# Performance work log

Hardware: AMD Instinct MI355X
Metric: run time of the kernel (lower is better)

## Reference

```python
import jax, jax.numpy as jnp
import numpy as np

# Module hyperparameters (from init_kwargs)
KERNEL = (16, 16)     # sliding window shape; Linear in_features = prod = 256
STRIDE = (8, 8)       # window stride
DILATION = (4, 4)     # per-window output tile; Linear out_features = prod = 16
# padding = 0, bias = False (module defaults)


def setup_inputs() -> dict:
    key = jax.random.key(0)
    k1, k2 = jax.random.split(key)
    x = jax.random.normal(k1, (32, 1024, 1024), dtype=jnp.float32)
    # torch nn.Linear weight convention: [out_features, in_features] = [16, 256]
    weight = jax.random.normal(k2, (16, 256), dtype=jnp.float32) / 16.0  # ~1/sqrt(in)
    return {"x": x, "weight": weight}


def reference(x, weight):
    # im2col: extract all sliding windows, flattened in (kh, kw) row-major order
    # (matches torch's window.flatten() since there is a single implicit channel).
    B = x.shape[0]
    patches = jax.lax.conv_general_dilated_patches(
        x[:, None],                 # [B, 1, H, W]
        filter_shape=KERNEL,
        window_strides=STRIDE,
        padding='VALID',
    )                               # [B, prod(KERNEL)=256, nH=127, nW=127]
    nH, nW = patches.shape[2], patches.shape[3]
    d0, d1 = DILATION
    # Dense per-patch linear: y = W @ flat_window   (bias=False)
    out = jnp.einsum('bkij,ok->bijo', patches, weight)   # [B, nH, nW, 16]
    # Each patch's 16 outputs reshape to a (4,4) tile placed at its output site.
    out = out.reshape(B, nH, nW, d0, d1)
    out = out.transpose(0, 1, 3, 2, 4).reshape(B, nH * d0, nW * d1)  # [B, 508, 508]
    return out
```

## Files before the change

### kernel.cpp

```cpp
#include <hip/hip_runtime.h>


typedef __attribute__((ext_vector_type(8))) short short8;
typedef __attribute__((ext_vector_type(4))) float f32x4;

#define ROWS 72
#define ROWG 33
#define NG   (ROWS * ROWG)

__device__ __forceinline__ unsigned pk2(float a, float b) {
    unsigned r;
    asm("v_cvt_pk_bf16_f32 %0, %1, %2" : "=v"(r) : "v"(a), "v"(b));
    return r;
}

__global__ __launch_bounds__(512, 4)
void conv_mfma3(const float* __restrict__ x,
                const float* __restrict__ w,
                float* __restrict__ out) {
    __shared__ uint4 lds[NG];

    const int tid  = threadIdx.x;
    const int lane = tid & 63;
    const int wv   = tid >> 6;
    const int bx   = blockIdx.x;
    const int st   = bx & 3;
    const int i0   = (bx >> 2) * 8;
    const int b    = blockIdx.y;

    const float* xb = x + (size_t)b * (1024 * 1024);
    const int basecol = st * 256;
    const int jb      = st * 32;

    const int o = lane & 15;
    short8 wfrag[8];
    #pragma unroll
    for (int s = 0; s < 8; ++s) {
        const float* wp = w + o * 256 + s * 32 + (lane >> 4) * 8;
        float4 w0 = *(const float4*)wp;
        float4 w1 = *(const float4*)(wp + 4);
        uint4 f = make_uint4(pk2(w0.x, w0.y), pk2(w0.z, w0.w),
                             pk2(w1.x, w1.y), pk2(w1.z, w1.w));
        wfrag[s] = __builtin_bit_cast(short8, f);
    }

    for (int g = tid; g < NG; g += 512) {
        int row = g / ROWG;
        int c8  = g - row * ROWG;
        int grow = i0 * 8 + row;      if (grow > 1023) grow = 1023;
        int gcol = basecol + c8 * 8;  if (gcol > 1016) gcol = 1016;
        const float* src = xb + grow * 1024 + gcol;
        float4 v0 = *(const float4*)src;
        float4 v1 = *(const float4*)(src + 4);
        lds[g] = make_uint4(pk2(v0.x, v0.y), pk2(v0.z, v0.w),
                            pk2(v1.x, v1.y), pk2(v1.z, v1.w));
    }
    __syncthreads();

    const int m  = lane & 15;
    const int kb = (lane >> 4) & 1;
    const int hi = lane >> 5;
    const int p  = lane >> 4;
    const int ip = i0 + wv;
    const int g0 = (wv * 8 + hi) * ROWG + m + kb;

    #pragma unroll
    for (int jt = 0; jt < 2; ++jt) {
        f32x4 acc = {0.f, 0.f, 0.f, 0.f};
        #pragma unroll
        for (int s = 0; s < 8; ++s) {
            short8 a = *(const short8*)&lds[g0 + s * (2 * ROWG) + jt * 16];
            acc = __builtin_amdgcn_mfma_f32_16x16x32_bf16(wfrag[s], a, acc, 0, 0, 0);
        }
        const int jp = jb + jt * 16 + m;
        if (ip < 127 && jp < 127) {
            float* op = out + (size_t)b * (508 * 508) + (ip * 4 + p) * 508 + jp * 4;
            *(float4*)op = *(float4*)&acc;
        }
    }
}

extern "C" void kernel_launch(void* const* d_in, const int* in_sizes, int n_in,
                              void* d_out, int out_size, void* d_ws, size_t ws_size,
                              hipStream_t stream) {
    const float* x = (const float*)d_in[0];
    const float* w = (const float*)d_in[1];
    float* out = (float*)d_out;
    dim3 grid(64, 32);
    conv_mfma3<<<grid, dim3(512, 1, 1), 0, stream>>>(x, w, out);
}
```

Baseline: 48.47 us.

## Retile conv to 136x136 tiles with batched global loads and four accumulators per wave

Each block now covers a square 128x128 input region (136 rows by 17 groups of 8 columns) instead of a 72-row by 256-column strip, and runs 256 threads with each wave producing four output rows of patches. Every thread issues all of its global loads into registers before any bf16 conversion or LDS store, so more memory requests are in flight at once. The weight fragment load now happens after the tile loads. The square tile lowers the halo overhead per output relative to the strip, but it raises register pressure from the 18 float4 staging values, and the LDS tile stays about the same size while the thread count per block is halved.

```diff
diff --git a/kernel.cpp b/kernel.cpp
--- a/kernel.cpp
+++ b/kernel.cpp
@@ -4,9 +4,9 @@
 typedef __attribute__((ext_vector_type(8))) short short8;
 typedef __attribute__((ext_vector_type(4))) float f32x4;
 
-#define ROWS 72
-#define ROWG 33
-#define NG   (ROWS * ROWG)
+#define NGR   17
+#define NROWS 136
+#define NG    (NROWS * NGR)
 
 __device__ __forceinline__ unsigned pk2(float a, float b) {
     unsigned r;
@@ -14,8 +14,13 @@
     return r;
 }
 
-__global__ __launch_bounds__(512, 4)
-void conv_mfma3(const float* __restrict__ x,
+__device__ __forceinline__ uint4 cvt8(float4 v0, float4 v1) {
+    return make_uint4(pk2(v0.x, v0.y), pk2(v0.z, v0.w),
+                      pk2(v1.x, v1.y), pk2(v1.z, v1.w));
+}
+
+__global__ __launch_bounds__(256, 4)
+void conv_mfma4(const float* __restrict__ x,
                 const float* __restrict__ w,
                 float* __restrict__ out) {
     __shared__ uint4 lds[NG];
@@ -24,13 +29,42 @@
     const int lane = tid & 63;
     const int wv   = tid >> 6;
     const int bx   = blockIdx.x;
-    const int st   = bx & 3;
-    const int i0   = (bx >> 2) * 8;
+    const int jt   = bx & 7;
+    const int it   = bx >> 3;
     const int b    = blockIdx.y;
 
     const float* xb = x + (size_t)b * (1024 * 1024);
-    const int basecol = st * 256;
-    const int jb      = st * 32;
+    const int baserow = it * 128;
+    const int basecol = jt * 128;
+
+    float4 vt0, vt1;
+    const bool tail = (tid < 8);
+    if (tail) {
+        int g = 2304 + tid;
+        int c8 = g - 135 * NGR;
+        int gr = baserow + 135; if (gr > 1023) gr = 1023;
+        int gc = basecol + c8 * 8; if (gc > 1016) gc = 1016;
+        const float4* s = (const float4*)(xb + gr * 1024 + gc);
+        vt0 = s[0]; vt1 = s[1];
+    }
+    float4 va[18];
+    #pragma unroll
+    for (int i2 = 0; i2 < 9; ++i2) {
+        int g   = tid + i2 * 256;
+        int row = g / NGR;
+        int c8  = g - row * NGR;
+        int gr  = baserow + row;     if (gr > 1023) gr = 1023;
+        int gc  = basecol + c8 * 8;  if (gc > 1016) gc = 1016;
+        const float4* s = (const float4*)(xb + gr * 1024 + gc);
+        va[i2 * 2]     = s[0];
+        va[i2 * 2 + 1] = s[1];
+    }
+
+    #pragma unroll
+    for (int i2 = 0; i2 < 9; ++i2) {
+        lds[tid + i2 * 256] = cvt8(va[i2 * 2], va[i2 * 2 + 1]);
+    }
+    if (tail) lds[2304 + tid] = cvt8(vt0, vt1);
 
     const int o = lane & 15;
     short8 wfrag[8];
@@ -39,43 +73,40 @@
         const float* wp = w + o * 256 + s * 32 + (lane >> 4) * 8;
         float4 w0 = *(const float4*)wp;
         float4 w1 = *(const float4*)(wp + 4);
-        uint4 f = make_uint4(pk2(w0.x, w0.y), pk2(w0.z, w0.w),
-                             pk2(w1.x, w1.y), pk2(w1.z, w1.w));
-        wfrag[s] = __builtin_bit_cast(short8, f);
-    }
-
-    for (int g = tid; g < NG; g += 512) {
-        int row = g / ROWG;
-        int c8  = g - row * ROWG;
-        int grow = i0 * 8 + row;      if (grow > 1023) grow = 1023;
-        int gcol = basecol + c8 * 8;  if (gcol > 1016) gcol = 1016;
-        const float* src = xb + grow * 1024 + gcol;
-        float4 v0 = *(const float4*)src;
-        float4 v1 = *(const float4*)(src + 4);
-        lds[g] = make_uint4(pk2(v0.x, v0.y), pk2(v0.z, v0.w),
-                            pk2(v1.x, v1.y), pk2(v1.z, v1.w));
+        wfrag[s] = __builtin_bit_cast(short8, cvt8(w0, w1));
     }
     __syncthreads();
 
     const int m  = lane & 15;
     const int kb = (lane >> 4) & 1;
     const int hi = lane >> 5;
-    const int p  = lane >> 4;
-    const int ip = i0 + wv;
-    const int g0 = (wv * 8 + hi) * ROWG + m + kb;
+    const unsigned short* lbase =
+        (const unsigned short*)lds + ((wv * 32 + hi) * NGR + m + kb) * 8;
+
+    f32x4 acc[4];
+    #pragma unroll
+    for (int t = 0; t < 4; ++t) acc[t] = (f32x4){0.f, 0.f, 0.f, 0.f};
 
     #pragma unroll
-    for (int jt = 0; jt < 2; ++jt) {
-        f32x4 acc = {0.f, 0.f, 0.f, 0.f};
-        #pragma unroll
-        for (int s = 0; s < 8; ++s) {
-            short8 a = *(const short8*)&lds[g0 + s * (2 * ROWG) + jt * 16];
-            acc = __builtin_amdgcn_mfma_f32_16x16x32_bf16(wfrag[s], a, acc, 0, 0, 0);
-        }
-        const int jp = jb + jt * 16 + m;
+    for (int s = 0; s < 8; ++s) {
+        short8 a0 = *(const short8*)(lbase + s * 272 + 0 * 1088);
+        short8 a1 = *(const short8*)(lbase + s * 272 + 1 * 1088);
+        short8 a2 = *(const short8*)(lbase + s * 272 + 2 * 1088);
+        short8 a3 = *(const short8*)(lbase + s * 272 + 3 * 1088);
+        acc[0] = __builtin_amdgcn_mfma_f32_16x16x32_bf16(wfrag[s], a0, acc[0], 0, 0, 0);
+        acc[1] = __builtin_amdgcn_mfma_f32_16x16x32_bf16(wfrag[s], a1, acc[1], 0, 0, 0);
+        acc[2] = __builtin_amdgcn_mfma_f32_16x16x32_bf16(wfrag[s], a2, acc[2], 0, 0, 0);
+        acc[3] = __builtin_amdgcn_mfma_f32_16x16x32_bf16(wfrag[s], a3, acc[3], 0, 0, 0);
+    }
+
+    const int p  = lane >> 4;
+    const int jp = jt * 16 + m;
+    #pragma unroll
+    for (int t = 0; t < 4; ++t) {
+        const int ip = it * 16 + wv * 4 + t;
         if (ip < 127 && jp < 127) {
             float* op = out + (size_t)b * (508 * 508) + (ip * 4 + p) * 508 + jp * 4;
-            *(float4*)op = *(float4*)&acc;
+            *(float4*)op = *(float4*)&acc[t];
         }
     }
 }
@@ -87,5 +118,5 @@
     const float* w = (const float*)d_in[1];
     float* out = (float*)d_out;
     dim3 grid(64, 32);
-    conv_mfma3<<<grid, dim3(512, 1, 1), 0, stream>>>(x, w, out);
+    conv_mfma4<<<grid, dim3(256, 1, 1), 0, stream>>>(x, w, out);
 }
```

Result: faster. 44.41 us (-8.4%).

## Replace LDS-staged tile with direct per-lane global loads feeding MFMA

Applied to the files above, without the earlier changes.

Removes the shared-memory staging of the input tile and the block barrier; each lane now loads its window rows directly from global memory into registers and converts them to bf16 before the MFMA. Block size drops to 256 threads and each wave loops over four patch rows, with a new grid mapping of column and row tiles. The packed hardware bf16 convert is replaced with a manual rounding routine. This trades LDS traffic and synchronisation for redundant global/L2 reads of overlapping windows and extra ALU work in the conversion.

```diff
diff --git a/kernel.cpp b/kernel.cpp
--- a/kernel.cpp
+++ b/kernel.cpp
@@ -4,75 +4,76 @@
 typedef __attribute__((ext_vector_type(8))) short short8;
 typedef __attribute__((ext_vector_type(4))) float f32x4;
 
-#define ROWS 72
-#define ROWG 33
-#define NG   (ROWS * ROWG)
+__device__ __forceinline__ unsigned short f2bf(float f) {
+    unsigned int u = __builtin_bit_cast(unsigned int, f);
+    u = (u + 0x7fffu + ((u >> 16) & 1u)) >> 16;
+    return (unsigned short)u;
+}
 
-__device__ __forceinline__ unsigned pk2(float a, float b) {
-    unsigned r;
-    asm("v_cvt_pk_bf16_f32 %0, %1, %2" : "=v"(r) : "v"(a), "v"(b));
+__device__ __forceinline__ short8 cvt8c(float4 v0, float4 v1) {
+    short8 r;
+    r[0] = (short)f2bf(v0.x); r[1] = (short)f2bf(v0.y);
+    r[2] = (short)f2bf(v0.z); r[3] = (short)f2bf(v0.w);
+    r[4] = (short)f2bf(v1.x); r[5] = (short)f2bf(v1.y);
+    r[6] = (short)f2bf(v1.z); r[7] = (short)f2bf(v1.w);
     return r;
 }
 
-__global__ __launch_bounds__(512, 4)
-void conv_mfma3(const float* __restrict__ x,
-                const float* __restrict__ w,
-                float* __restrict__ out) {
-    __shared__ uint4 lds[NG];
-
+__global__ __launch_bounds__(256, 4)
+void conv_direct2(const float* __restrict__ x,
+                  const float* __restrict__ w,
+                  float* __restrict__ out) {
     const int tid  = threadIdx.x;
     const int lane = tid & 63;
     const int wv   = tid >> 6;
     const int bx   = blockIdx.x;
-    const int st   = bx & 3;
-    const int i0   = (bx >> 2) * 8;
+    const int jt   = bx & 7;
+    const int it   = bx >> 3;
     const int b    = blockIdx.y;
 
     const float* xb = x + (size_t)b * (1024 * 1024);
-    const int basecol = st * 256;
-    const int jb      = st * 32;
-
-    const int o = lane & 15;
-    short8 wfrag[8];
-    #pragma unroll
-    for (int s = 0; s < 8; ++s) {
-        const float* wp = w + o * 256 + s * 32 + (lane >> 4) * 8;
-        float4 w0 = *(const float4*)wp;
-        float4 w1 = *(const float4*)(wp + 4);
-        uint4 f = make_uint4(pk2(w0.x, w0.y), pk2(w0.z, w0.w),
-                             pk2(w1.x, w1.y), pk2(w1.z, w1.w));
-        wfrag[s] = __builtin_bit_cast(short8, f);
-    }
-
-    for (int g = tid; g < NG; g += 512) {
-        int row = g / ROWG;
-        int c8  = g - row * ROWG;
-        int grow = i0 * 8 + row;      if (grow > 1023) grow = 1023;
-        int gcol = basecol + c8 * 8;  if (gcol > 1016) gcol = 1016;
-        const float* src = xb + grow * 1024 + gcol;
-        float4 v0 = *(const float4*)src;
-        float4 v1 = *(const float4*)(src + 4);
-        lds[g] = make_uint4(pk2(v0.x, v0.y), pk2(v0.z, v0.w),
-                            pk2(v1.x, v1.y), pk2(v1.z, v1.w));
-    }
-    __syncthreads();
 
     const int m  = lane & 15;
     const int kb = (lane >> 4) & 1;
     const int hi = lane >> 5;
     const int p  = lane >> 4;
-    const int ip = i0 + wv;
-    const int g0 = (wv * 8 + hi) * ROWG + m + kb;
 
+    short8 wfrag[8];
     #pragma unroll
-    for (int jt = 0; jt < 2; ++jt) {
+    for (int s = 0; s < 8; ++s) {
+        const float* wp = w + m * 256 + s * 32 + (lane >> 4) * 8;
+        float4 w0 = *(const float4*)wp;
+        float4 w1 = *(const float4*)(wp + 4);
+        wfrag[s] = cvt8c(w0, w1);
+    }
+
+    int colf = jt * 128 + m * 8 + kb * 8;
+    if (colf > 1016) colf = 1016;
+    const int loff = hi * 1024 + colf;
+    const int jp   = jt * 16 + m;
+
+    #pragma unroll 1
+    for (int t = 0; t < 4; ++t) {
+        const int ip = it * 16 + wv * 4 + t;
+        int r0 = ip * 8;
+        if (r0 > 1008) r0 = 1008;
+        const float* base = xb + (size_t)r0 * 1024 + loff;
+
+        float4 lv[16];
+        #pragma unroll
+        for (int s = 0; s < 8; ++s) {
+            const float* rp = base + s * 2048;
+            lv[2 * s]     = *(const float4*)rp;
+            lv[2 * s + 1] = *(const float4*)(rp + 4);
+        }
+
         f32x4 acc = {0.f, 0.f, 0.f, 0.f};
         #pragma unroll
         for (int s = 0; s < 8; ++s) {
-            short8 a = *(const short8*)&lds[g0 + s * (2 * ROWG) + jt * 16];
-            acc = __builtin_amdgcn_mfma_f32_16x16x32_bf16(wfrag[s], a, acc, 0, 0, 0);
+            short8 bfr = cvt8c(lv[2 * s], lv[2 * s + 1]);
+            acc = __builtin_amdgcn_mfma_f32_16x16x32_bf16(wfrag[s], bfr, acc, 0, 0, 0);
         }
-        const int jp = jb + jt * 16 + m;
+
         if (ip < 127 && jp < 127) {
             float* op = out + (size_t)b * (508 * 508) + (ip * 4 + p) * 508 + jp * 4;
             *(float4*)op = *(float4*)&acc;
@@ -87,5 +88,5 @@
     const float* w = (const float*)d_in[1];
     float* out = (float*)d_out;
     dim3 grid(64, 32);
-    conv_mfma3<<<grid, dim3(512, 1, 1), 0, stream>>>(x, w, out);
+    conv_direct2<<<grid, dim3(256, 1, 1), 0, stream>>>(x, w, out);
 }
```

After: 53.33 us. 1.1x slower.
